# Optimization experiments

Measured on AMD Instinct MI355X. Metric: run time of the kernel, lower is better.

Reference implementation:

```python
import jax, jax.numpy as jnp
import numpy as np

EPS = 1e-12  # F.normalize eps


def _l2norm_c(x):
    # normalize over channel dim (axis=1), matching F.normalize(dim=1)
    n = jnp.sqrt(jnp.sum(x * x, axis=1, keepdims=True))
    return x / jnp.maximum(n, EPS)


def _rotate_all(q, angles_deg):
    """Rotate q [B,C,H,W] by every angle in angles_deg [A] via affine_grid +
    bilinear grid_sample (align_corners=False, zeros padding). Returns [A,B,C,H,W]."""
    B, C, H, W = q.shape
    th = jnp.deg2rad(angles_deg)
    # affine_grid align_corners=False output normalized coords
    xn = (2.0 * jnp.arange(W, dtype=q.dtype) + 1.0) / W - 1.0  # [W]
    yn = (2.0 * jnp.arange(H, dtype=q.dtype) + 1.0) / H - 1.0  # [H]
    c = jnp.cos(th)[:, None, None]
    s = jnp.sin(th)[:, None, None]
    gx = c * xn[None, None, :] - s * yn[None, :, None]  # [A,H,W]
    gy = s * xn[None, None, :] + c * yn[None, :, None]  # [A,H,W]
    # grid_sample align_corners=False: normalized -> input pixel coords
    ix = ((gx + 1.0) * W - 1.0) * 0.5
    iy = ((gy + 1.0) * H - 1.0) * 0.5
    x0 = jnp.floor(ix)
    y0 = jnp.floor(iy)
    wx = ix - x0  # frac weights
    wy = iy - y0
    x0i = x0.astype(jnp.int32)
    y0i = y0.astype(jnp.int32)

    def corner(yi, xi, w):
        valid = (xi >= 0) & (xi < W) & (yi >= 0) & (yi < H)  # zeros padding
        xc = jnp.clip(xi, 0, W - 1)
        yc = jnp.clip(yi, 0, H - 1)
        vals = q[:, :, yc, xc]  # advanced indexing -> [B,C,A,H,W]
        return vals * (w * valid.astype(q.dtype))[None, None]

    out = (corner(y0i, x0i, (1.0 - wx) * (1.0 - wy))
           + corner(y0i, x0i + 1, wx * (1.0 - wy))
           + corner(y0i + 1, x0i, (1.0 - wx) * wy)
           + corner(y0i + 1, x0i + 1, wx * wy))  # [B,C,A,H,W]
    return jnp.transpose(out, (2, 0, 1, 3, 4))  # [A,B,C,H,W]


def setup_inputs() -> dict:
    key = jax.random.key(0)
    ks = jax.random.split(key, 6)
    B, Cin, H, W, HID, A = 8, 768, 32, 32, 128, 36
    gallery_map = jax.random.normal(ks[0], (B, Cin, H, W), jnp.float32)
    query_map = jax.random.normal(ks[1], (B, Cin, H, W), jnp.float32)
    angles_deg = jnp.arange(A, dtype=jnp.float32) * 10.0 - 180.0
    Wg = jax.random.normal(ks[2], (HID, Cin), jnp.float32) / np.float32(np.sqrt(Cin))
    Wq = jax.random.normal(ks[3], (HID, Cin), jnp.float32) / np.float32(np.sqrt(Cin))
    W1 = jax.random.normal(ks[4], (HID, 4 * HID), jnp.float32) / np.float32(np.sqrt(4 * HID))
    b1 = jnp.zeros((HID,), jnp.float32)
    W2 = jax.random.normal(ks[5], (1, HID), jnp.float32) / np.float32(np.sqrt(HID))
    b2 = jnp.zeros((1,), jnp.float32)
    return {"gallery_map": gallery_map, "query_map": query_map, "Wg": Wg, "Wq": Wq,
            "W1": W1, "b1": b1, "W2": W2, "b2": b2, "angles_deg": angles_deg}


def reference(gallery_map, query_map, Wg, Wq, W1, b1, W2, b2, angles_deg):
    # 1x1-conv projections + channel L2 normalization (encode)
    g = _l2norm_c(jnp.einsum('oc,bchw->bohw', Wg, gallery_map))  # [B,HID,H,W]
    q = _l2norm_c(jnp.einsum('oc,bchw->bohw', Wq, query_map))    # [B,HID,H,W]
    qr = _rotate_all(q, angles_deg)  # [A,B,HID,H,W]
    HID = W1.shape[0]
    # head conv1 over cat([g, qr, g*qr, |g-qr|]) == sum of 4 block matmuls
    W1g, W1q, W1m, W1a = (W1[:, :HID], W1[:, HID:2 * HID],
                          W1[:, 2 * HID:3 * HID], W1[:, 3 * HID:])
    base = jnp.einsum('oc,bchw->bohw', W1g, g)  # angle-independent term
    h = (base[None]
         + jnp.einsum('oc,abchw->abohw', W1q, qr)
         + jnp.einsum('oc,abchw->abohw', W1m, g[None] * qr)
         + jnp.einsum('oc,abchw->abohw', W1a, jnp.abs(g[None] - qr))
         + b1[None, None, :, None, None])
    h = jax.nn.relu(h)  # [A,B,HID,H,W]
    H_, W_ = h.shape[-2], h.shape[-1]
    # head conv2 (HID->1) + spatial mean pool, per angle
    logits = jnp.einsum('c,abchw->ab', W2[0], h) / (H_ * W_) + b2[0]  # [A,B]
    return logits.T  # [B,A] matching torch.stack(logits, dim=1)
```

## Files before the change

### kernel.cpp

```cpp
#include <hip/hip_runtime.h>
#include <math.h>

#define B_   8
#define CIN  768
#define HID  128
#define NA   36
#define PP   1024

typedef _Float16 f16;
typedef __attribute__((ext_vector_type(2))) _Float16 f16x2;
typedef __attribute__((ext_vector_type(4))) _Float16 f16x4;
typedef __attribute__((ext_vector_type(8))) _Float16 f16x8;
typedef __attribute__((ext_vector_type(4))) float f32x4;
typedef __attribute__((ext_vector_type(4))) unsigned short us4;

#define MFMA16(a, b, c) __builtin_amdgcn_mfma_f32_16x16x32_f16((a), (b), (c), 0, 0, 0)

__device__ inline f16x2 pkrtz(float a, float b) {
  union { __fp16 __attribute__((ext_vector_type(2))) r; f16x2 h; } u;
  u.r = __builtin_amdgcn_cvt_pkrtz(a, b);
  return u.h;
}

__device__ inline void rot_corners(float ct, float st, int y, int x,
                                   float w[4], int p[4]) {
  float xn = (2.0f * x + 1.0f) * (1.0f / 32.0f) - 1.0f;
  float yn = (2.0f * y + 1.0f) * (1.0f / 32.0f) - 1.0f;
  float gx = ct * xn - st * yn;
  float gy = st * xn + ct * yn;
  float ix = ((gx + 1.0f) * 32.0f - 1.0f) * 0.5f;
  float iy = ((gy + 1.0f) * 32.0f - 1.0f) * 0.5f;
  float x0f = floorf(ix), y0f = floorf(iy);
  float wx = ix - x0f, wy = iy - y0f;
  int x0 = (int)x0f, y0 = (int)y0f;
  int x1 = x0 + 1, y1 = y0 + 1;
  float vx0 = (x0 >= 0 && x0 < 32) ? 1.0f : 0.0f;
  float vx1 = (x1 >= 0 && x1 < 32) ? 1.0f : 0.0f;
  float vy0 = (y0 >= 0 && y0 < 32) ? 1.0f : 0.0f;
  float vy1 = (y1 >= 0 && y1 < 32) ? 1.0f : 0.0f;
  int cx0 = min(max(x0, 0), 31), cx1 = min(max(x1, 0), 31);
  int cy0 = min(max(y0, 0), 31), cy1 = min(max(y1, 0), 31);
  w[0] = (1.0f - wx) * (1.0f - wy) * vx0 * vy0;  p[0] = (cy0 << 5) + cx0;
  w[1] = wx * (1.0f - wy) * vx1 * vy0;           p[1] = (cy0 << 5) + cx1;
  w[2] = (1.0f - wx) * wy * vx0 * vy1;           p[2] = (cy1 << 5) + cx0;
  w[3] = wx * wy * vx1 * vy1;                    p[3] = (cy1 << 5) + cx1;
}

__global__ __launch_bounds__(256) void prep_k(
    const float* __restrict__ Wg, const float* __restrict__ Wq,
    const float* __restrict__ W1, const float* __restrict__ b2,
    f16* __restrict__ Wg_h, f16* __restrict__ Wq_h,
    f16* __restrict__ W1_h, float* __restrict__ out) {
  int idx = blockIdx.x * 256 + threadIdx.x;
  if (idx < B_ * NA) out[idx] = b2[0];
  if (idx < 32768) {
    int e = idx * 8;
    const float* src; f16* dst; int off;
    if (e < 98304)       { src = Wg; dst = Wg_h; off = e; }
    else if (e < 196608) { src = Wq; dst = Wq_h; off = e - 98304; }
    else                 { src = W1; dst = W1_h; off = e - 196608; }
    float4 lo = *(const float4*)(src + off);
    float4 hi = *(const float4*)(src + off + 4);
    f16x8 h;
    h[0] = (f16)lo.x; h[1] = (f16)lo.y; h[2] = (f16)lo.z; h[3] = (f16)lo.w;
    h[4] = (f16)hi.x; h[5] = (f16)hi.y; h[6] = (f16)hi.z; h[7] = (f16)hi.w;
    *(f16x8*)(dst + off) = h;
  }
}

#define WCH_S 264
#define PS_S  132
#define GN_S  136
__global__ __launch_bounds__(512, 4) void projfused_k(
    const float* __restrict__ gal, const float* __restrict__ qry,
    const f16* __restrict__ Wg_h, const f16* __restrict__ Wq_h,
    const f16* __restrict__ W1_h, const float* __restrict__ b1,
    f16* __restrict__ gout, f16* __restrict__ qout,
    float* __restrict__ baseb1) {
  __shared__ __align__(16) char LDSU[67584];
  f16*   Wch = (f16*)LDSU;
  float* ps  = (float*)LDSU;
  f16*   Gn  = (f16*)LDSU;
  f16*   W1l = (f16*)(LDSU + 8704);

  int pblk = blockIdx.x, b = blockIdx.y, z = blockIdx.z;
  const float* imgB = (z ? qry : gal) + (size_t)b * CIN * PP;
  const f16* Wm = z ? Wq_h : Wg_h;
  f16* dst = z ? qout : gout;
  int tid = threadIdx.x, lane = tid & 63, wv = tid >> 6;
  int q = lane >> 4, lr = lane & 15;
  int kw = wv & 3, mw = wv >> 2;
  int pw = pblk * 32 + mw * 16;

  f32x4 acc[8];
  #pragma unroll
  for (int t = 0; t < 8; t++) acc[t] = (f32x4){0.f, 0.f, 0.f, 0.f};

  int so = tid >> 2, sseg = (tid & 3) * 64;
  const float* ipb = imgB + (size_t)(kw * 64 + q * 8) * PP + pw + lr;

  float fim[2][16];
  #pragma unroll
  for (int t = 0; t < 16; t++)
    fim[0][t] = ipb[(size_t)((t >> 3) * 32 + (t & 7)) * PP];

  #pragma unroll
  for (int c3 = 0; c3 < 3; c3++) {
    int cc = c3 << 8;
    f16x8 w8[8];
    #pragma unroll
    for (int j = 0; j < 8; j++)
      w8[j] = *(const f16x8*)(Wm + so * CIN + cc + sseg + j * 8);
    if (c3 < 2) {
      #pragma unroll
      for (int t = 0; t < 16; t++)
        fim[(c3 + 1) & 1][t] =
            ipb[(size_t)(((c3 + 1) << 8) + (t >> 3) * 32 + (t & 7)) * PP];
    }
    #pragma unroll
    for (int j = 0; j < 8; j++)
      *(f16x8*)&Wch[so * WCH_S + sseg + j * 8] = w8[j];
    __syncthreads();
    #pragma unroll
    for (int ksi = 0; ksi < 2; ksi++) {
      union { f16x8 v; f16x2 h[4]; } bf;
      const float* fp = &fim[c3 & 1][ksi * 8];
      bf.h[0] = pkrtz(fp[0], fp[1]); bf.h[1] = pkrtz(fp[2], fp[3]);
      bf.h[2] = pkrtz(fp[4], fp[5]); bf.h[3] = pkrtz(fp[6], fp[7]);
      int k0 = kw * 64 + ksi * 32;
      #pragma unroll
      for (int og = 0; og < 8; og++) {
        f16x8 af = *(const f16x8*)&Wch[(og * 16 + lr) * WCH_S + k0 + q * 8];
        acc[og] = MFMA16(af, bf.v, acc[og]);
      }
    }
    __syncthreads();
  }

  #pragma unroll
  for (int og = 0; og < 8; og++)
    *(f32x4*)&ps[kw * (32 * PS_S) + (mw * 16 + lr) * PS_S + og * 16 + q * 4] = acc[og];
  __syncthreads();
  int pos = tid >> 4, oo = (tid & 15) * 8;
  f32x4 v0s = (f32x4){0.f,0.f,0.f,0.f}, v1s = (f32x4){0.f,0.f,0.f,0.f};
  #pragma unroll
  for (int k = 0; k < 4; k++) {
    v0s += *(const f32x4*)&ps[k * (32 * PS_S) + pos * PS_S + oo];
    v1s += *(const f32x4*)&ps[k * (32 * PS_S) + pos * PS_S + oo + 4];
  }
  float ss = v0s.x*v0s.x + v0s.y*v0s.y + v0s.z*v0s.z + v0s.w*v0s.w
           + v1s.x*v1s.x + v1s.y*v1s.y + v1s.z*v1s.z + v1s.w*v1s.w;
  ss += __shfl_xor(ss, 1); ss += __shfl_xor(ss, 2);
  ss += __shfl_xor(ss, 4); ss += __shfl_xor(ss, 8);
  float inv = 1.0f / fmaxf(sqrtf(ss), 1e-12f);
  f16x8 gn8;
  gn8[0] = (f16)(v0s.x*inv); gn8[1] = (f16)(v0s.y*inv);
  gn8[2] = (f16)(v0s.z*inv); gn8[3] = (f16)(v0s.w*inv);
  gn8[4] = (f16)(v1s.x*inv); gn8[5] = (f16)(v1s.y*inv);
  gn8[6] = (f16)(v1s.z*inv); gn8[7] = (f16)(v1s.w*inv);
  *(f16x8*)(dst + (size_t)((b << 10) + pblk * 32 + pos) * HID + oo) = gn8;

  if (z == 0) {
    __syncthreads();
    *(f16x8*)&Gn[pos * GN_S + oo] = gn8;
    {
      int o = tid >> 2, seg = (tid & 3) * 32;
      #pragma unroll
      for (int j = 0; j < 4; j++)
        *(f16x8*)&W1l[o * GN_S + seg + j * 8] =
            *(const f16x8*)(W1_h + o * 512 + seg + j * 8);
    }
    __syncthreads();
    int nw = wv & 3, mw2 = wv >> 2;
    f32x4 acc2[2];
    acc2[0] = (f32x4){0.f,0.f,0.f,0.f}; acc2[1] = (f32x4){0.f,0.f,0.f,0.f};
    #pragma unroll
    for (int ksj = 0; ksj < 4; ksj++) {
      f16x8 bfv = *(const f16x8*)&Gn[(mw2 * 16 + lr) * GN_S + ksj * 32 + q * 8];
      #pragma unroll
      for (int og2 = 0; og2 < 2; og2++) {
        f16x8 af = *(const f16x8*)&W1l[(nw * 32 + og2 * 16 + lr) * GN_S + ksj * 32 + q * 8];
        acc2[og2] = MFMA16(af, bfv, acc2[og2]);
      }
    }
    #pragma unroll
    for (int og2 = 0; og2 < 2; og2++) {
      int o0 = nw * 32 + og2 * 16 + q * 4;
      float4 bb = *(const float4*)(b1 + o0);
      float4 r;
      r.x = acc2[og2][0] + bb.x; r.y = acc2[og2][1] + bb.y;
      r.z = acc2[og2][2] + bb.z; r.w = acc2[og2][3] + bb.w;
      *(float4*)(baseb1 + (size_t)((b << 10) + pblk * 32 + mw2 * 16 + lr) * HID + o0) = r;
    }
  }
}

__global__ __launch_bounds__(256, 2) void main_k(
    const f16* __restrict__ g_h, const f16* __restrict__ q_h,
    const float* __restrict__ baseb1, const f16* __restrict__ W1_h,
    const float* __restrict__ W2, const float* __restrict__ angles,
    float* __restrict__ out) {
  __shared__ f16 Xs[2][32 * 392];
  __shared__ f16 wtab[6][32][4];
  __shared__ unsigned short ptab[6][32][4];
  __shared__ float redl[24];
  int y = blockIdx.x, b = blockIdx.y;
  int tid = threadIdx.x;
  int lane = tid & 63, wv = tid >> 6;
  int q = lane >> 4, lr = lane & 15;
  int nq = wv * 32;

  if (tid < 192) {
    int it = tid >> 5, pos = tid & 31;
    float th = angles[blockIdx.z * 6 + it] * 0.017453292519943295f;
    float ct = cosf(th), st = sinf(th);
    float w4[4]; int p4[4];
    rot_corners(ct, st, y, pos, w4, p4);
    f16x4 wh;
    wh[0] = (f16)w4[0]; wh[1] = (f16)w4[1];
    wh[2] = (f16)w4[2]; wh[3] = (f16)w4[3];
    *(f16x4*)&wtab[it][pos][0] = wh;
    us4 ph;
    ph[0] = (unsigned short)p4[0]; ph[1] = (unsigned short)p4[1];
    ph[2] = (unsigned short)p4[2]; ph[3] = (unsigned short)p4[3];
    *(us4*)&ptab[it][pos][0] = ph;
  }

  f16x8 bfr[12][2];
  #pragma unroll
  for (int s = 0; s < 12; s++)
    #pragma unroll
    for (int ni = 0; ni < 2; ni++) {
      int o = nq + ni * 16 + lr;
      bfr[s][ni] = *(const f16x8*)(W1_h + o * 512 + 128 + s * 32 + q * 8);
    }

  float w2v[2];
  #pragma unroll
  for (int ni = 0; ni < 2; ni++) w2v[ni] = W2[nq + ni * 16 + lr];

  f32x4 binit[2][2];
  #pragma unroll
  for (int mi = 0; mi < 2; mi++)
    #pragma unroll
    for (int ni = 0; ni < 2; ni++)
      #pragma unroll
      for (int r = 0; r < 4; r++) {
        int m = mi * 16 + q * 4 + r;
        binit[mi][ni][r] =
            baseb1[(size_t)((b << 10) + (y << 5) + m) * HID + nq + ni * 16 + lr];
      }

  int bx = tid >> 3, ks = tid & 7;
  const f16* qB = q_h + ((size_t)(b << 10)) * HID + ks * 16;
  const f16* gB = g_h + (size_t)((b << 10) + (y << 5) + bx) * HID + ks * 16;
  f16x8 gg[2] = { *(const f16x8*)gB, *(const f16x8*)(gB + 8) };

  __syncthreads();

  f16x8 u[2][2][4];
  f16x4 wcur, wnxt;
  {
    wcur = *(const f16x4*)&wtab[0][bx][0];
    us4 pt = *(const us4*)&ptab[0][bx][0];
    #pragma unroll
    for (int cg = 0; cg < 2; cg++) {
      u[0][cg][0] = *(const f16x8*)(qB + (int)pt[0] * HID + cg * 8);
      u[0][cg][1] = *(const f16x8*)(qB + (int)pt[1] * HID + cg * 8);
      u[0][cg][2] = *(const f16x8*)(qB + (int)pt[2] * HID + cg * 8);
      u[0][cg][3] = *(const f16x8*)(qB + (int)pt[3] * HID + cg * 8);
    }
  }

  float spart[6];
  #pragma unroll
  for (int it = 0; it < 6; it++) {
    int cur = it & 1;
    f16* Xb = &Xs[cur][0];
    {
      f16x2 wc[4];
      wc[0] = (f16x2){wcur[0], wcur[0]};
      wc[1] = (f16x2){wcur[1], wcur[1]};
      wc[2] = (f16x2){wcur[2], wcur[2]};
      wc[3] = (f16x2){wcur[3], wcur[3]};
      #pragma unroll
      for (int cg = 0; cg < 2; cg++) {
        int c = ks * 16 + cg * 8;
        union U8 { f16x8 v; f16x2 h[4]; } u0, u1, u2, u3, gv, oq, om, oa;
        u0.v = u[cur][cg][0]; u1.v = u[cur][cg][1];
        u2.v = u[cur][cg][2]; u3.v = u[cur][cg][3];
        gv.v = gg[cg];
        #pragma unroll
        for (int i = 0; i < 4; i++) {
          f16x2 qr = u0.h[i] * wc[0] + u1.h[i] * wc[1]
                   + u2.h[i] * wc[2] + u3.h[i] * wc[3];
          f16x2 mm = gv.h[i] * qr;
          union { f16x2 h; unsigned int uu; } dd;
          dd.h = gv.h[i] - qr;
          dd.uu &= 0x7fff7fffu;
          oq.h[i] = qr; om.h[i] = mm; oa.h[i] = dd.h;
        }
        *(f16x8*)&Xb[bx * 392 + c] = oq.v;
        *(f16x8*)&Xb[bx * 392 + 128 + c] = om.v;
        *(f16x8*)&Xb[bx * 392 + 256 + c] = oa.v;
      }
    }
    if (it < 5) {
      wnxt = *(const f16x4*)&wtab[it + 1][bx][0];
      us4 pt = *(const us4*)&ptab[it + 1][bx][0];
      #pragma unroll
      for (int cg = 0; cg < 2; cg++) {
        u[cur ^ 1][cg][0] = *(const f16x8*)(qB + (int)pt[0] * HID + cg * 8);
        u[cur ^ 1][cg][1] = *(const f16x8*)(qB + (int)pt[1] * HID + cg * 8);
        u[cur ^ 1][cg][2] = *(const f16x8*)(qB + (int)pt[2] * HID + cg * 8);
        u[cur ^ 1][cg][3] = *(const f16x8*)(qB + (int)pt[3] * HID + cg * 8);
      }
    }
    __syncthreads();

    f32x4 a00 = binit[0][0], a01 = binit[0][1];
    f32x4 a10 = binit[1][0], a11 = binit[1][1];
    #pragma unroll
    for (int s = 0; s < 12; s++) {
      f16x8 af0 = *(const f16x8*)&Xb[(lr) * 392 + s * 32 + q * 8];
      f16x8 af1 = *(const f16x8*)&Xb[(16 + lr) * 392 + s * 32 + q * 8];
      a00 = MFMA16(af0, bfr[s][0], a00);
      a01 = MFMA16(af0, bfr[s][1], a01);
      a10 = MFMA16(af1, bfr[s][0], a10);
      a11 = MFMA16(af1, bfr[s][1], a11);
    }

    float sv = 0.f;
    #pragma unroll
    for (int r = 0; r < 4; r++) {
      sv = fmaf(w2v[0], fmaxf(a00[r], 0.f), sv);
      sv = fmaf(w2v[1], fmaxf(a01[r], 0.f), sv);
      sv = fmaf(w2v[0], fmaxf(a10[r], 0.f), sv);
      sv = fmaf(w2v[1], fmaxf(a11[r], 0.f), sv);
    }
    spart[it] = sv;
    wcur = wnxt;
  }

  #pragma unroll
  for (int it = 0; it < 6; it++) {
    float v = spart[it];
    #pragma unroll
    for (int off = 32; off > 0; off >>= 1) v += __shfl_down(v, off, 64);
    if (lane == 0) redl[wv * 6 + it] = v;
  }
  __syncthreads();
  if (tid < 6) {
    float tot = redl[tid] + redl[6 + tid] + redl[12 + tid] + redl[18 + tid];
    atomicAdd(&out[b * NA + blockIdx.z * 6 + tid], tot * (1.0f / 1024.0f));
  }
}

extern "C" void kernel_launch(void* const* d_in, const int* in_sizes, int n_in,
                              void* d_out, int out_size, void* d_ws, size_t ws_size,
                              hipStream_t stream) {
  const float* gal = (const float*)d_in[0];
  const float* qry = (const float*)d_in[1];
  const float* Wg  = (const float*)d_in[2];
  const float* Wq  = (const float*)d_in[3];
  const float* W1  = (const float*)d_in[4];
  const float* b1  = (const float*)d_in[5];
  const float* W2  = (const float*)d_in[6];
  const float* b2  = (const float*)d_in[7];
  const float* ang = (const float*)d_in[8];
  float* out = (float*)d_out;
  char* ws = (char*)d_ws;
  f16*   g_h    = (f16*)ws;
  f16*   q_h    = (f16*)(ws + (2u << 20));
  float* baseb1 = (float*)(ws + (4u << 20));
  f16*   Wg_h   = (f16*)(ws + (8u << 20));
  f16*   Wq_h   = (f16*)(ws + (8u << 20) + 196608);
  f16*   W1_h   = (f16*)(ws + (8u << 20) + 393216);

  hipLaunchKernelGGL(prep_k, dim3(128), dim3(256), 0, stream,
                     Wg, Wq, W1, b2, Wg_h, Wq_h, W1_h, out);
  hipLaunchKernelGGL(projfused_k, dim3(32, 8, 2), dim3(512), 0, stream,
                     gal, qry, Wg_h, Wq_h, W1_h, b1, g_h, q_h, baseb1);
  hipLaunchKernelGGL(main_k, dim3(32, 8, 6), dim3(256), 0, stream,
                     g_h, q_h, baseb1, W1_h, W2, ang, out);
}
```

Measured before the change: 158.7 us.

## Fold weight prep into projection kernel and restructure main loop into paired angles

Drops the separate prep_k launch. The projection kernel now converts fp32 Wg/Wq/W1 to fp16 while loading, initialises the output with b2, and has its z=1 blocks write the fp16 copy of W1 for main_k. In main_k the per-thread cache of W1 B-fragments and the register-prefetched corner values are gone. Angles are now processed two at a time into both LDS buffers, with W1 fragments read from global inside the MFMA loop, to cut register pressure and the kernel launch. The trade-off is more global and LDS loads per MFMA, an extra barrier per angle pair, and the W1 weights being converted again in every projection block.

Result: slower. 199.3 us (+25.6%).

```diff
diff --git a/kernel.cpp b/kernel.cpp
--- a/kernel.cpp
+++ b/kernel.cpp
@@ -20,6 +20,13 @@
   union { __fp16 __attribute__((ext_vector_type(2))) r; f16x2 h; } u;
   u.r = __builtin_amdgcn_cvt_pkrtz(a, b);
   return u.h;
+}
+
+__device__ inline f16x8 cvt8_rne(float4 lo, float4 hi) {
+  f16x8 h;
+  h[0] = (f16)lo.x; h[1] = (f16)lo.y; h[2] = (f16)lo.z; h[3] = (f16)lo.w;
+  h[4] = (f16)hi.x; h[5] = (f16)hi.y; h[6] = (f16)hi.z; h[7] = (f16)hi.w;
+  return h;
 }
 
 __device__ inline void rot_corners(float ct, float st, int y, int x,
@@ -46,37 +53,17 @@
   w[3] = wx * wy * vx1 * vy1;                    p[3] = (cy1 << 5) + cx1;
 }
 
-__global__ __launch_bounds__(256) void prep_k(
-    const float* __restrict__ Wg, const float* __restrict__ Wq,
-    const float* __restrict__ W1, const float* __restrict__ b2,
-    f16* __restrict__ Wg_h, f16* __restrict__ Wq_h,
-    f16* __restrict__ W1_h, float* __restrict__ out) {
-  int idx = blockIdx.x * 256 + threadIdx.x;
-  if (idx < B_ * NA) out[idx] = b2[0];
-  if (idx < 32768) {
-    int e = idx * 8;
-    const float* src; f16* dst; int off;
-    if (e < 98304)       { src = Wg; dst = Wg_h; off = e; }
-    else if (e < 196608) { src = Wq; dst = Wq_h; off = e - 98304; }
-    else                 { src = W1; dst = W1_h; off = e - 196608; }
-    float4 lo = *(const float4*)(src + off);
-    float4 hi = *(const float4*)(src + off + 4);
-    f16x8 h;
-    h[0] = (f16)lo.x; h[1] = (f16)lo.y; h[2] = (f16)lo.z; h[3] = (f16)lo.w;
-    h[4] = (f16)hi.x; h[5] = (f16)hi.y; h[6] = (f16)hi.z; h[7] = (f16)hi.w;
-    *(f16x8*)(dst + off) = h;
-  }
-}
-
 #define WCH_S 264
 #define PS_S  132
 #define GN_S  136
 __global__ __launch_bounds__(512, 4) void projfused_k(
     const float* __restrict__ gal, const float* __restrict__ qry,
-    const f16* __restrict__ Wg_h, const f16* __restrict__ Wq_h,
-    const f16* __restrict__ W1_h, const float* __restrict__ b1,
+    const float* __restrict__ Wg, const float* __restrict__ Wq,
+    const float* __restrict__ W1, const float* __restrict__ b1,
+    const float* __restrict__ b2,
     f16* __restrict__ gout, f16* __restrict__ qout,
-    float* __restrict__ baseb1) {
+    float* __restrict__ baseb1, f16* __restrict__ W1_h,
+    float* __restrict__ out) {
   __shared__ __align__(16) char LDSU[67584];
   f16*   Wch = (f16*)LDSU;
   float* ps  = (float*)LDSU;
@@ -85,13 +72,15 @@
 
   int pblk = blockIdx.x, b = blockIdx.y, z = blockIdx.z;
   const float* imgB = (z ? qry : gal) + (size_t)b * CIN * PP;
-  const f16* Wm = z ? Wq_h : Wg_h;
+  const float* Wm32 = z ? Wq : Wg;
   f16* dst = z ? qout : gout;
   int tid = threadIdx.x, lane = tid & 63, wv = tid >> 6;
   int q = lane >> 4, lr = lane & 15;
   int kw = wv & 3, mw = wv >> 2;
   int pw = pblk * 32 + mw * 16;
 
+  if (z == 0 && b == 0 && pblk == 0 && tid < B_ * NA) out[tid] = b2[0];
+
   f32x4 acc[8];
   #pragma unroll
   for (int t = 0; t < 8; t++) acc[t] = (f32x4){0.f, 0.f, 0.f, 0.f};
@@ -109,8 +98,10 @@
     int cc = c3 << 8;
     f16x8 w8[8];
     #pragma unroll
-    for (int j = 0; j < 8; j++)
-      w8[j] = *(const f16x8*)(Wm + so * CIN + cc + sseg + j * 8);
+    for (int j = 0; j < 8; j++) {
+      const float* wp = Wm32 + (size_t)so * CIN + cc + sseg + j * 8;
+      w8[j] = cvt8_rne(*(const float4*)wp, *(const float4*)(wp + 4));
+    }
     if (c3 < 2) {
       #pragma unroll
       for (int t = 0; t < 16; t++)
@@ -166,9 +157,11 @@
     {
       int o = tid >> 2, seg = (tid & 3) * 32;
       #pragma unroll
-      for (int j = 0; j < 4; j++)
+      for (int j = 0; j < 4; j++) {
+        const float* wp = W1 + (size_t)o * 512 + seg + j * 8;
         *(f16x8*)&W1l[o * GN_S + seg + j * 8] =
-            *(const f16x8*)(W1_h + o * 512 + seg + j * 8);
+            cvt8_rne(*(const float4*)wp, *(const float4*)(wp + 4));
+      }
     }
     __syncthreads();
     int nw = wv & 3, mw2 = wv >> 2;
@@ -191,6 +184,12 @@
       r.x = acc2[og2][0] + bb.x; r.y = acc2[og2][1] + bb.y;
       r.z = acc2[og2][2] + bb.z; r.w = acc2[og2][3] + bb.w;
       *(float4*)(baseb1 + (size_t)((b << 10) + pblk * 32 + mw2 * 16 + lr) * HID + o0) = r;
+    }
+  } else {
+    if (tid < 128) {
+      int e = ((b * 32 + pblk) * 128 + tid) * 2;
+      *(f16x2*)(W1_h + e) = pkrtz(0.f, 0.f),
+      *(f16x2*)(W1_h + e) = (f16x2){(f16)W1[e], (f16)W1[e + 1]};
     }
   }
 }
@@ -226,15 +225,6 @@
     *(us4*)&ptab[it][pos][0] = ph;
   }
 
-  f16x8 bfr[12][2];
-  #pragma unroll
-  for (int s = 0; s < 12; s++)
-    #pragma unroll
-    for (int ni = 0; ni < 2; ni++) {
-      int o = nq + ni * 16 + lr;
-      bfr[s][ni] = *(const f16x8*)(W1_h + o * 512 + 128 + s * 32 + q * 8);
-    }
-
   float w2v[2];
   #pragma unroll
   for (int ni = 0; ni < 2; ni++) w2v[ni] = W2[nq + ni * 16 + lr];
@@ -256,39 +246,37 @@
   const f16* gB = g_h + (size_t)((b << 10) + (y << 5) + bx) * HID + ks * 16;
   f16x8 gg[2] = { *(const f16x8*)gB, *(const f16x8*)(gB + 8) };
 
+  const f16* w1p0 = W1_h + (size_t)(nq + lr) * 512 + 128 + q * 8;
+  const f16* w1p1 = W1_h + (size_t)(nq + 16 + lr) * 512 + 128 + q * 8;
+
   __syncthreads();
 
-  f16x8 u[2][2][4];
-  f16x4 wcur, wnxt;
-  {
-    wcur = *(const f16x4*)&wtab[0][bx][0];
-    us4 pt = *(const us4*)&ptab[0][bx][0];
-    #pragma unroll
-    for (int cg = 0; cg < 2; cg++) {
-      u[0][cg][0] = *(const f16x8*)(qB + (int)pt[0] * HID + cg * 8);
-      u[0][cg][1] = *(const f16x8*)(qB + (int)pt[1] * HID + cg * 8);
-      u[0][cg][2] = *(const f16x8*)(qB + (int)pt[2] * HID + cg * 8);
-      u[0][cg][3] = *(const f16x8*)(qB + (int)pt[3] * HID + cg * 8);
-    }
-  }
-
   float spart[6];
   #pragma unroll
-  for (int it = 0; it < 6; it++) {
-    int cur = it & 1;
-    f16* Xb = &Xs[cur][0];
-    {
+  for (int ph2 = 0; ph2 < 3; ph2++) {
+    #pragma unroll
+    for (int half = 0; half < 2; half++) {
+      int it = ph2 * 2 + half;
+      f16* Xb = &Xs[half][0];
+      f16x4 wq4 = *(const f16x4*)&wtab[it][bx][0];
+      us4 pt = *(const us4*)&ptab[it][bx][0];
       f16x2 wc[4];
-      wc[0] = (f16x2){wcur[0], wcur[0]};
-      wc[1] = (f16x2){wcur[1], wcur[1]};
-      wc[2] = (f16x2){wcur[2], wcur[2]};
-      wc[3] = (f16x2){wcur[3], wcur[3]};
+      wc[0] = (f16x2){wq4[0], wq4[0]};
+      wc[1] = (f16x2){wq4[1], wq4[1]};
+      wc[2] = (f16x2){wq4[2], wq4[2]};
+      wc[3] = (f16x2){wq4[3], wq4[3]};
+      const f16* c0p = qB + (int)pt[0] * HID;
+      const f16* c1p = qB + (int)pt[1] * HID;
+      const f16* c2p = qB + (int)pt[2] * HID;
+      const f16* c3p = qB + (int)pt[3] * HID;
       #pragma unroll
       for (int cg = 0; cg < 2; cg++) {
         int c = ks * 16 + cg * 8;
         union U8 { f16x8 v; f16x2 h[4]; } u0, u1, u2, u3, gv, oq, om, oa;
-        u0.v = u[cur][cg][0]; u1.v = u[cur][cg][1];
-        u2.v = u[cur][cg][2]; u3.v = u[cur][cg][3];
+        u0.v = *(const f16x8*)(c0p + cg * 8);
+        u1.v = *(const f16x8*)(c1p + cg * 8);
+        u2.v = *(const f16x8*)(c2p + cg * 8);
+        u3.v = *(const f16x8*)(c3p + cg * 8);
         gv.v = gg[cg];
         #pragma unroll
         for (int i = 0; i < 4; i++) {
@@ -305,41 +293,41 @@
         *(f16x8*)&Xb[bx * 392 + 256 + c] = oa.v;
       }
     }
-    if (it < 5) {
-      wnxt = *(const f16x4*)&wtab[it + 1][bx][0];
-      us4 pt = *(const us4*)&ptab[it + 1][bx][0];
-      #pragma unroll
-      for (int cg = 0; cg < 2; cg++) {
-        u[cur ^ 1][cg][0] = *(const f16x8*)(qB + (int)pt[0] * HID + cg * 8);
-        u[cur ^ 1][cg][1] = *(const f16x8*)(qB + (int)pt[1] * HID + cg * 8);
-        u[cur ^ 1][cg][2] = *(const f16x8*)(qB + (int)pt[2] * HID + cg * 8);
-        u[cur ^ 1][cg][3] = *(const f16x8*)(qB + (int)pt[3] * HID + cg * 8);
-      }
-    }
-    __syncthreads();
-
-    f32x4 a00 = binit[0][0], a01 = binit[0][1];
-    f32x4 a10 = binit[1][0], a11 = binit[1][1];
+    __syncthreads();
+
+    f32x4 aA00 = binit[0][0], aA01 = binit[0][1];
+    f32x4 aA10 = binit[1][0], aA11 = binit[1][1];
+    f32x4 aB00 = binit[0][0], aB01 = binit[0][1];
+    f32x4 aB10 = binit[1][0], aB11 = binit[1][1];
     #pragma unroll
     for (int s = 0; s < 12; s++) {
-      f16x8 af0 = *(const f16x8*)&Xb[(lr) * 392 + s * 32 + q * 8];
-      f16x8 af1 = *(const f16x8*)&Xb[(16 + lr) * 392 + s * 32 + q * 8];
-      a00 = MFMA16(af0, bfr[s][0], a00);
-      a01 = MFMA16(af0, bfr[s][1], a01);
-      a10 = MFMA16(af1, bfr[s][0], a10);
-      a11 = MFMA16(af1, bfr[s][1], a11);
-    }
-
-    float sv = 0.f;
+      f16x8 b0  = *(const f16x8*)(w1p0 + s * 32);
+      f16x8 b1v = *(const f16x8*)(w1p1 + s * 32);
+      f16x8 fA0 = *(const f16x8*)&Xs[0][(lr) * 392 + s * 32 + q * 8];
+      f16x8 fA1 = *(const f16x8*)&Xs[0][(16 + lr) * 392 + s * 32 + q * 8];
+      f16x8 fB0 = *(const f16x8*)&Xs[1][(lr) * 392 + s * 32 + q * 8];
+      f16x8 fB1 = *(const f16x8*)&Xs[1][(16 + lr) * 392 + s * 32 + q * 8];
+      aA00 = MFMA16(fA0, b0, aA00);  aA01 = MFMA16(fA0, b1v, aA01);
+      aA10 = MFMA16(fA1, b0, aA10);  aA11 = MFMA16(fA1, b1v, aA11);
+      aB00 = MFMA16(fB0, b0, aB00);  aB01 = MFMA16(fB0, b1v, aB01);
+      aB10 = MFMA16(fB1, b0, aB10);  aB11 = MFMA16(fB1, b1v, aB11);
+    }
+
+    float svA = 0.f, svB = 0.f;
     #pragma unroll
     for (int r = 0; r < 4; r++) {
-      sv = fmaf(w2v[0], fmaxf(a00[r], 0.f), sv);
-      sv = fmaf(w2v[1], fmaxf(a01[r], 0.f), sv);
-      sv = fmaf(w2v[0], fmaxf(a10[r], 0.f), sv);
-      sv = fmaf(w2v[1], fmaxf(a11[r], 0.f), sv);
-    }
-    spart[it] = sv;
-    wcur = wnxt;
+      svA = fmaf(w2v[0], fmaxf(aA00[r], 0.f), svA);
+      svA = fmaf(w2v[1], fmaxf(aA01[r], 0.f), svA);
+      svA = fmaf(w2v[0], fmaxf(aA10[r], 0.f), svA);
+      svA = fmaf(w2v[1], fmaxf(aA11[r], 0.f), svA);
+      svB = fmaf(w2v[0], fmaxf(aB00[r], 0.f), svB);
+      svB = fmaf(w2v[1], fmaxf(aB01[r], 0.f), svB);
+      svB = fmaf(w2v[0], fmaxf(aB10[r], 0.f), svB);
+      svB = fmaf(w2v[1], fmaxf(aB11[r], 0.f), svB);
+    }
+    spart[ph2 * 2]     = svA;
+    spart[ph2 * 2 + 1] = svB;
+    __syncthreads();
   }
 
   #pragma unroll
@@ -373,14 +361,10 @@
   f16*   g_h    = (f16*)ws;
   f16*   q_h    = (f16*)(ws + (2u << 20));
   float* baseb1 = (float*)(ws + (4u << 20));
-  f16*   Wg_h   = (f16*)(ws + (8u << 20));
-  f16*   Wq_h   = (f16*)(ws + (8u << 20) + 196608);
-  f16*   W1_h   = (f16*)(ws + (8u << 20) + 393216);
-
-  hipLaunchKernelGGL(prep_k, dim3(128), dim3(256), 0, stream,
-                     Wg, Wq, W1, b2, Wg_h, Wq_h, W1_h, out);
+  f16*   W1_h   = (f16*)(ws + (8u << 20));
+
   hipLaunchKernelGGL(projfused_k, dim3(32, 8, 2), dim3(512), 0, stream,
-                     gal, qry, Wg_h, Wq_h, W1_h, b1, g_h, q_h, baseb1);
+                     gal, qry, Wg, Wq, W1, b1, b2, g_h, q_h, baseb1, W1_h, out);
   hipLaunchKernelGGL(main_k, dim3(32, 8, 6), dim3(256), 0, stream,
                      g_h, q_h, baseb1, W1_h, W2, ang, out);
 }
```
